# Optimization experiments

Hardware: AMD Instinct MI355X
Metric: run time of the kernel (lower is better)

Reference implementation:

```python
import jax, jax.numpy as jnp
import numpy as np
import math

B = 2
D_MODEL = 2048
L_MAX = 4096
FILTER_ORDER = 64
EMB_DIM = 3
SHORT_K = 3


def setup_inputs() -> dict:
    key = jax.random.key(0)
    ks = jax.random.split(key, 16)
    D = D_MODEL

    def n(k, shape, scale=0.02):
        return jax.random.normal(k, shape, dtype=jnp.float32) * scale

    return {
        "x": jax.random.normal(ks[0], (B, L_MAX, D), dtype=jnp.float32),
        "in_proj_w": n(ks[1], (3 * D, D)),
        "in_proj_b": n(ks[2], (3 * D,)),
        "short_w": n(ks[3], (3 * D, 1, SHORT_K), 0.3),   # depthwise conv weight (O, I/groups=1, K)
        "short_b": n(ks[4], (3 * D,), 0.1),
        "mlp_w0": n(ks[5], (FILTER_ORDER, EMB_DIM), 0.5),
        "mlp_b0": n(ks[6], (FILTER_ORDER,), 0.5),
        "sin_freq": jnp.ones((1, FILTER_ORDER), dtype=jnp.float32),  # Sin module, w=1, shared across MLP layers
        "mlp_w1": n(ks[7], (FILTER_ORDER, FILTER_ORDER), 0.1),
        "mlp_b1": n(ks[8], (FILTER_ORDER,), 0.1),
        "mlp_w2": n(ks[9], (FILTER_ORDER, FILTER_ORDER), 0.1),
        "mlp_b2": n(ks[10], (FILTER_ORDER,), 0.1),
        "mlp_w3": n(ks[11], (D, FILTER_ORDER), 0.1),      # final Linear(order -> d_model, bias=False)
        "filter_bias": jax.random.normal(ks[12], (D,), dtype=jnp.float32),  # HyenaFilter.bias ~ randn
        "out_proj_w": n(ks[13], (D, D)),
        "out_proj_b": n(ks[14], (D,)),
    }


def _pos_emb(L):
    # PositionalEmbedding: t in [0,1], 1 complex band (emb_dim=3 -> bands=1)
    t = jnp.linspace(0.0, 1.0, L)[:, None]               # (L, 1)
    t_resc = jnp.linspace(0.0, L - 1.0, L)
    w = 2.0 * math.pi * t_resc / L                       # (L,)
    bands = (EMB_DIM - 1) // 2
    f = jnp.linspace(1e-4, bands - 1.0, bands)           # (bands,)
    ang = f[None, :] * w[:, None]                        # (L, bands)
    # z = exp(-1j * f * w) -> real = cos, imag = -sin
    z = jnp.concatenate([t, jnp.cos(ang), -jnp.sin(ang)], axis=-1)  # (L, 3)
    return z, t


def _filter_k(L, w0, b0, freq, w1, b1, w2, b2, w3):
    z, t = _pos_emb(L)
    h = jnp.sin(freq * (z @ w0.T + b0))
    h = jnp.sin(freq * (h @ w1.T + b1))
    h = jnp.sin(freq * (h @ w2.T + b2))
    h = h @ w3.T                                         # (L, D)
    # ExponentialModulation: deltas = linspace(log(.01)/1.5, log(.01)/0.3, D)
    max_decay = math.log(0.01) / 0.3
    min_decay = math.log(0.01) / 1.5
    deltas = jnp.linspace(min_decay, max_decay, h.shape[-1])
    decay = jnp.exp(-t * jnp.abs(deltas)[None, :])       # (L, D)
    return (h * decay).T                                 # (D, L)


def _fftconv(u, k, bias):
    # fftconv_ref with gelu=False, no dropout_mask: u (B, D, L), k (D, L), bias (D,)
    L = u.shape[-1]
    n = 2 * L
    k_f = jnp.fft.rfft(k, n=n) / n                       # (D, L+1)
    u_f = jnp.fft.rfft(u, n=n)                           # (B, D, L+1)
    y = jnp.fft.irfft(u_f * k_f, n=n, norm="forward")[..., :L]
    return y + u * bias[:, None]


def reference(x, in_proj_w, in_proj_b, short_w, short_b, mlp_w0, mlp_b0, sin_freq,
              mlp_w1, mlp_b1, mlp_w2, mlp_b2, mlp_w3, filter_bias,
              out_proj_w, out_proj_b):
    Bn, L, D = x.shape
    u = x @ in_proj_w.T + in_proj_b                      # (B, L, 3D)
    u = jnp.transpose(u, (0, 2, 1))                      # (B, 3D, L)
    # depthwise short conv, padding = short_k - 1, truncate to L (causal-ish)
    uc = jax.lax.conv_general_dilated(
        u, short_w, window_strides=(1,),
        padding=[(SHORT_K - 1, SHORT_K - 1)],
        feature_group_count=3 * D,
        dimension_numbers=("NCH", "OIH", "NCH"))
    uc = uc[..., :L] + short_b[None, :, None]
    x0, x1, v = jnp.split(uc, 3, axis=1)                 # each (B, D, L)
    k = _filter_k(L, mlp_w0, mlp_b0, sin_freq, mlp_w1, mlp_b1, mlp_w2, mlp_b2, mlp_w3)
    # order=2 Hyena recurrence: single gated long-conv step
    v = v * x1
    v = _fftconv(v, k, filter_bias)
    y = v * x0                                           # (B, D, L)
    y = jnp.transpose(y, (0, 2, 1))                      # (B, L, D)
    return y @ out_proj_w.T + out_proj_b
```

## Files before the change

kernel.cpp:

```cpp
#include <hip/hip_runtime.h>
#include <hip/hip_bf16.h>
#include <cstdint>
#include <cstddef>

typedef __attribute__((ext_vector_type(8))) short    bf16x8;
typedef __attribute__((ext_vector_type(4))) float    f32x4;
typedef __attribute__((ext_vector_type(8))) unsigned short u16x8;
typedef __attribute__((ext_vector_type(4))) float    f32v4;
typedef __attribute__((ext_vector_type(4))) unsigned short u16v4;

__device__ __forceinline__ float b2f(unsigned short v) {
    return __builtin_bit_cast(float, ((unsigned int)v) << 16);
}
__device__ __forceinline__ unsigned short f2b(float f) {
    unsigned int u = __builtin_bit_cast(unsigned int, f);
    u += 0x7fffu + ((u >> 16) & 1u);
    return (unsigned short)(u >> 16);
}

__device__ __forceinline__ void async16(const void* g, void* l) {
    __builtin_amdgcn_global_load_lds(
        (const __attribute__((address_space(1))) unsigned int*)g,
        (__attribute__((address_space(3))) unsigned int*)l, 16, 0, 0);
}

__global__ __launch_bounds__(256) void cvt_f32_bf16(const float* __restrict__ src,
                                                    unsigned short* __restrict__ dst, int n4) {
    int i = blockIdx.x * blockDim.x + threadIdx.x;
    int stride = gridDim.x * blockDim.x;
    const f32v4* s4 = (const f32v4*)src;
    u16v4* d4 = (u16v4*)dst;
    for (; i < n4; i += stride) {
        f32v4 v = s4[i];
        u16v4 o;
        o.x = f2b(v.x); o.y = f2b(v.y); o.z = f2b(v.z); o.w = f2b(v.w);
        d4[i] = o;
    }
}

template <int MODE>
__global__ __launch_bounds__(512, 1) void gemm256(
    const unsigned short* __restrict__ A,
    const unsigned short* __restrict__ Bw,
    const float* __restrict__ bias,
    void* __restrict__ Cout,
    int M, int N, int K, int Lseq, int CH, int ntn)
{
    constexpr int SMEM_BYTES = (MODE == 1) ? 135168 : 131072;
    __shared__ char smemc[SMEM_BYTES];

    const int tid = threadIdx.x;
    const int w   = tid >> 6;
    const int l   = tid & 63;
    const int wm  = w & 1;
    const int wn  = w >> 1;
    const int quad = l >> 4;
    const int lq   = l & 15;

    int id = blockIdx.x;
    const int q8 = gridDim.x >> 3;
    id = (id & 7) * q8 + (id >> 3);
    const int bx = id % ntn, by = id / ntn;
    const int n0 = bx * 256, m0 = by * 256;

    const int su0 = quad ^ (lq & 7);
    const int su1 = su0 ^ 4;

    uint32_t offAe[2][2], offBe[2][2];
    int dA[2][2], dB[2][2];
    #pragma unroll
    for (int h = 0; h < 2; ++h)
        #pragma unroll
        for (int c = 0; c < 2; ++c) {
            const int Lr = h * 128 + w * 16 + c * 8 + (l >> 3);
            const int gA = ((Lr & 64) << 1) | ((Lr & 128) >> 1) | (Lr & 63);
            const int u  = (l & 7) ^ (l >> 3);
            offAe[h][c] = (uint32_t)(m0 + gA) * (uint32_t)K + (uint32_t)(u * 8);
            offBe[h][c] = (uint32_t)(n0 + Lr) * (uint32_t)K + (uint32_t)(u * 8);
            const int rb = (h * 128 + w * 16 + c * 8) * 128;
            dA[h][c] = rb;
            dB[h][c] = 32768 + rb;
        }

#define STAGE_A(bs, h, tile) do { \
    async16(A + offAe[h][0] + (size_t)(tile) * 64, smemc + ((bs) * 65536 + dA[h][0])); \
    async16(A + offAe[h][1] + (size_t)(tile) * 64, smemc + ((bs) * 65536 + dA[h][1])); \
} while (0)
#define STAGE_B(bs, h, tile) do { \
    async16(Bw + offBe[h][0] + (size_t)(tile) * 64, smemc + ((bs) * 65536 + dB[h][0])); \
    async16(Bw + offBe[h][1] + (size_t)(tile) * 64, smemc + ((bs) * 65536 + dB[h][1])); \
} while (0)

    f32x4 acc[8][4] = {};
    bf16x8 bw[4][2], a[2][2];

#define LDB8(bs) do { \
    _Pragma("unroll") for (int j = 0; j < 4; ++j) { \
        const int Lr = wn * 64 + j * 16 + lq; \
        bw[j][0] = *(const bf16x8*)(smemc + (bs) * 65536 + 32768 + Lr * 128 + su0 * 16); \
        bw[j][1] = *(const bf16x8*)(smemc + (bs) * 65536 + 32768 + Lr * 128 + su1 * 16); \
    } } while (0)
#define LDA4(bs, q) do { \
    _Pragma("unroll") for (int mf = 0; mf < 2; ++mf) { \
        const int g = wm * 128 + (q) * 32 + mf * 16 + lq; \
        const int Lr = ((g & 64) << 1) | ((g & 128) >> 1) | (g & 63); \
        a[mf][0] = *(const bf16x8*)(smemc + (bs) * 65536 + Lr * 128 + su0 * 16); \
        a[mf][1] = *(const bf16x8*)(smemc + (bs) * 65536 + Lr * 128 + su1 * 16); \
    } } while (0)
#define MFMA16(q) do { \
    _Pragma("unroll") for (int mf = 0; mf < 2; ++mf) \
    _Pragma("unroll") for (int j = 0; j < 4; ++j) \
    _Pragma("unroll") for (int kk = 0; kk < 2; ++kk) \
        acc[(q) * 2 + mf][j] = __builtin_amdgcn_mfma_f32_16x16x32_bf16(a[mf][kk], bw[j][kk], acc[(q) * 2 + mf][j], 0, 0, 0); \
} while (0)
#define PHASE_SYNC() do { \
    __builtin_amdgcn_s_barrier(); \
    asm volatile("s_waitcnt lgkmcnt(0)" ::: "memory"); \
    __builtin_amdgcn_sched_barrier(0); \
    __builtin_amdgcn_s_setprio(1); \
} while (0)
#define PHASE_END() do { \
    __builtin_amdgcn_s_setprio(0); \
    __builtin_amdgcn_s_barrier(); \
} while (0)
#define PHASE_END_DRAIN(lastf) do { \
    __builtin_amdgcn_s_setprio(0); \
    if (lastf) asm volatile("s_waitcnt vmcnt(0)" ::: "memory"); \
    else       asm volatile("s_waitcnt vmcnt(6)" ::: "memory"); \
    __builtin_amdgcn_s_barrier(); \
} while (0)

    STAGE_B(0, 0, 0); STAGE_B(0, 1, 0); STAGE_A(0, 0, 0); STAGE_A(0, 1, 0);
    STAGE_B(1, 0, 1); STAGE_B(1, 1, 1); STAGE_A(1, 0, 1);
    asm volatile("s_waitcnt vmcnt(6)" ::: "memory");
    __builtin_amdgcn_s_barrier();

    const int nIt = K >> 7;
    for (int i = 0; i < nIt; ++i) {
        const bool last = (i == nIt - 1);
        const int t0 = 2 * i, t1 = 2 * i + 1;
        LDB8(0); LDA4(0, 0); STAGE_A(1, 1, t1);
        PHASE_SYNC(); MFMA16(0); PHASE_END();
        LDA4(0, 1); if (!last) STAGE_B(0, 0, t0 + 2);
        PHASE_SYNC(); MFMA16(1); PHASE_END();
        LDA4(0, 2); if (!last) STAGE_B(0, 1, t0 + 2);
        PHASE_SYNC(); MFMA16(2); PHASE_END();
        LDA4(0, 3); if (!last) STAGE_A(0, 0, t0 + 2);
        PHASE_SYNC(); MFMA16(3); PHASE_END_DRAIN(last);
        LDB8(1); LDA4(1, 0); if (!last) STAGE_A(0, 1, t0 + 2);
        PHASE_SYNC(); MFMA16(0); PHASE_END();
        LDA4(1, 1); if (!last) STAGE_B(1, 0, t1 + 2);
        PHASE_SYNC(); MFMA16(1); PHASE_END();
        LDA4(1, 2); if (!last) STAGE_B(1, 1, t1 + 2);
        PHASE_SYNC(); MFMA16(2); PHASE_END();
        LDA4(1, 3); if (!last) STAGE_A(1, 0, t1 + 2);
        PHASE_SYNC(); MFMA16(3); PHASE_END_DRAIN(last);
    }

    if (MODE == 0) {
        float* out = (float*)Cout;
        #pragma unroll
        for (int j = 0; j < 4; ++j) {
            const int col = n0 + wn * 64 + j * 16 + lq;
            const float bv = bias[col];
            #pragma unroll
            for (int i8 = 0; i8 < 8; ++i8) {
                const int rowb = m0 + wm * 128 + i8 * 16 + quad * 4;
                f32x4 c = acc[i8][j];
                out[(size_t)(rowb + 0) * N + col] = c.x + bv;
                out[(size_t)(rowb + 1) * N + col] = c.y + bv;
                out[(size_t)(rowb + 2) * N + col] = c.z + bv;
                out[(size_t)(rowb + 3) * N + col] = c.w + bv;
            }
        }
    } else {
        unsigned short* sE = (unsigned short*)smemc;
        __syncthreads();
        #pragma unroll
        for (int j = 0; j < 4; ++j) {
            const int nl = wn * 64 + j * 16 + lq;
            const float bv = bias[n0 + nl];
            #pragma unroll
            for (int i8 = 0; i8 < 8; ++i8) {
                const int ml = wm * 128 + i8 * 16 + quad * 4;
                f32x4 c = acc[i8][j];
                u16v4 pk;
                pk.x = f2b(c.x + bv); pk.y = f2b(c.y + bv);
                pk.z = f2b(c.z + bv); pk.w = f2b(c.w + bv);
                *(u16v4*)&sE[nl * 264 + ml] = pk;
            }
        }
        __syncthreads();
        unsigned short* uo = (unsigned short*)Cout;
        const int bI = m0 >> 12;
        const int l0 = m0 & 4095;
        for (int e = tid; e < 8192; e += 512) {
            const int nl = e >> 5, seg = e & 31;
            u16x8 v = *(const u16x8*)&sE[nl * 264 + seg * 8];
            *(u16x8*)&uo[(size_t)(bI * CH + n0 + nl) * Lseq + l0 + seg * 8] = v;
        }
    }
#undef STAGE_A
#undef STAGE_B
#undef LDB8
#undef LDA4
#undef MFMA16
#undef PHASE_SYNC
#undef PHASE_END
#undef PHASE_END_DRAIN
}

__global__ __launch_bounds__(256) void filter_kernel(
    const float* __restrict__ w0, const float* __restrict__ b0,
    const float* __restrict__ freq,
    const float* __restrict__ w1, const float* __restrict__ b1,
    const float* __restrict__ w2, const float* __restrict__ b2,
    const float* __restrict__ w3, float* __restrict__ kf)
{
    __shared__ float ha[64][64];
    __shared__ float hb[64][64];
    const int tid = threadIdx.x;
    const int l0 = blockIdx.x * 64;
    const int d0 = blockIdx.y * 256;
    const int l  = tid & 63;
    const int lg = l0 + l;
    const float tt = (float)lg * (1.0f / 4095.0f);
    const float wang = 6.283185307179586f * (float)lg * (1.0f / 4096.0f);
    const float a  = 1e-4f * wang;
    const float z0 = tt, z1 = cosf(a), z2 = -sinf(a);

    for (int e = tid; e < 4096; e += 256) {
        const int dim = e >> 6;
        float pre = z0 * w0[dim * 3] + z1 * w0[dim * 3 + 1] + z2 * w0[dim * 3 + 2] + b0[dim];
        ha[dim][l] = sinf(freq[dim] * pre);
    }
    __syncthreads();
    for (int e = tid; e < 4096; e += 256) {
        const int dim = e >> 6;
        float acc = b1[dim];
        #pragma unroll
        for (int jj = 0; jj < 64; ++jj) acc += w1[dim * 64 + jj] * ha[jj][l];
        hb[dim][l] = sinf(freq[dim] * acc);
    }
    __syncthreads();
    for (int e = tid; e < 4096; e += 256) {
        const int dim = e >> 6;
        float acc = b2[dim];
        #pragma unroll
        for (int jj = 0; jj < 64; ++jj) acc += w2[dim * 64 + jj] * hb[jj][l];
        ha[dim][l] = sinf(freq[dim] * acc);
    }
    __syncthreads();
    for (int d = d0 + (tid >> 6); d < d0 + 256; d += 4) {
        float acc = 0.f;
        #pragma unroll
        for (int jj = 0; jj < 64; ++jj) acc += w3[d * 64 + jj] * ha[jj][l];
        const float delta = fabsf(-3.0701134573253944f + (-5.999245642062483e-3f) * (float)d);
        kf[(size_t)d * 4096 + lg] = acc * __expf(-tt * delta);
    }
}

#define PIDX(i) ((i) + (((i) >> 5) << 2))

__device__ __forceinline__ void bfly_f(float& r1, float& i1, float& r2, float& i2, float wr, float wi) {
    float ur = r1, ui = i1, vr = r2, vi = i2;
    r1 = ur + vr; i1 = ui + vi;
    float dr = ur - vr, di = ui - vi;
    r2 = dr * wr - di * wi;
    i2 = dr * wi + di * wr;
}
__device__ __forceinline__ void bfly_i(float& r1, float& i1, float& r2, float& i2, float wr, float wi) {
    float vr = r2 * wr - i2 * wi, vi = r2 * wi + i2 * wr;
    float ur = r1, ui = i1;
    r1 = ur + vr; i1 = ui + vi;
    r2 = ur - vr; i2 = ui - vi;
}

template <int DS, int STR>
__device__ __forceinline__ void fwd_stage(float* re, float* im, int tt) {
    float wr[8], wi[8];
    constexpr float c = -3.14159265358979f / (float)(STR * DS);
    #pragma unroll
    for (int k = 0; k < DS; ++k) __sincosf(c * (float)(tt + STR * k), &wi[k], &wr[k]);
    #pragma unroll
    for (int s = 0; s < 16; ++s)
        if ((s & DS) == 0)
            bfly_f(re[s], im[s], re[s + DS], im[s + DS], wr[s & (DS - 1)], wi[s & (DS - 1)]);
}
template <int DS, int STR>
__device__ __forceinline__ void inv_stage(float* re, float* im, int tt) {
    float wr[8], wi[8];
    constexpr float c = 3.14159265358979f / (float)(STR * DS);
    #pragma unroll
    for (int k = 0; k < DS; ++k) __sincosf(c * (float)(tt + STR * k), &wi[k], &wr[k]);
    #pragma unroll
    for (int s = 0; s < 16; ++s)
        if ((s & DS) == 0)
            bfly_i(re[s], im[s], re[s + DS], im[s + DS], wr[s & (DS - 1)], wi[s & (DS - 1)]);
}

__device__ __forceinline__ void xchg(float* re, float* im, float* fre, float* fim,
                                     int wbase, int wstr, int rbase, int rstr) {
    __syncthreads();
    if (wstr == 1) {
        #pragma unroll
        for (int q = 0; q < 4; ++q) {
            f32x4 vr, vi;
            vr.x = re[4*q+0]; vr.y = re[4*q+1]; vr.z = re[4*q+2]; vr.w = re[4*q+3];
            vi.x = im[4*q+0]; vi.y = im[4*q+1]; vi.z = im[4*q+2]; vi.w = im[4*q+3];
            *(f32x4*)&fre[PIDX(wbase + 4*q)] = vr;
            *(f32x4*)&fim[PIDX(wbase + 4*q)] = vi;
        }
    } else {
        #pragma unroll
        for (int s = 0; s < 16; ++s) {
            const int i = wbase + wstr * s;
            fre[PIDX(i)] = re[s]; fim[PIDX(i)] = im[s];
        }
    }
    __syncthreads();
    if (rstr == 1) {
        #pragma unroll
        for (int q = 0; q < 4; ++q) {
            f32x4 vr = *(const f32x4*)&fre[PIDX(rbase + 4*q)];
            f32x4 vi = *(const f32x4*)&fim[PIDX(rbase + 4*q)];
            re[4*q+0] = vr.x; re[4*q+1] = vr.y; re[4*q+2] = vr.z; re[4*q+3] = vr.w;
            im[4*q+0] = vi.x; im[4*q+1] = vi.y; im[4*q+2] = vi.z; im[4*q+3] = vi.w;
        }
    } else {
        #pragma unroll
        for (int s = 0; s < 16; ++s) {
            const int i = rbase + rstr * s;
            re[s] = fre[PIDX(i)]; im[s] = fim[PIDX(i)];
        }
    }
}

__device__ __forceinline__ void fwd_fft(float* re, float* im, float* fre, float* fim, int t) {
    const int off = t & 31, seg = t >> 5;
    fwd_stage<8, 512>(re, im, t);
    fwd_stage<4, 512>(re, im, t);
    fwd_stage<2, 512>(re, im, t);
    fwd_stage<1, 512>(re, im, t);
    xchg(re, im, fre, fim, t, 512, seg * 512 + off, 32);
    fwd_stage<8, 32>(re, im, off);
    fwd_stage<4, 32>(re, im, off);
    fwd_stage<2, 32>(re, im, off);
    fwd_stage<1, 32>(re, im, off);
    {
        float wr, wi;
        __sincosf(-3.14159265358979f * (float)(off & 15) / 16.0f, &wi, &wr);
        const bool hi = (off & 16) != 0;
        #pragma unroll
        for (int s = 0; s < 16; ++s) {
            float rr = __shfl_xor(re[s], 16);
            float ri = __shfl_xor(im[s], 16);
            if (!hi) { re[s] += rr; im[s] += ri; }
            else {
                float dr = rr - re[s], di = ri - im[s];
                re[s] = dr * wr - di * wi;
                im[s] = dr * wi + di * wr;
            }
        }
    }
    xchg(re, im, fre, fim, seg * 512 + off, 32, 16 * t, 1);
    fwd_stage<8, 1>(re, im, 0);
    fwd_stage<4, 1>(re, im, 0);
    fwd_stage<2, 1>(re, im, 0);
    fwd_stage<1, 1>(re, im, 0);
}

__device__ __forceinline__ void inv_fft(float* re, float* im, float* fre, float* fim, int t) {
    const int off = t & 31, seg = t >> 5;
    inv_stage<1, 1>(re, im, 0);
    inv_stage<2, 1>(re, im, 0);
    inv_stage<4, 1>(re, im, 0);
    inv_stage<8, 1>(re, im, 0);
    xchg(re, im, fre, fim, 16 * t, 1, seg * 512 + off, 32);
    {
        float wr, wi;
        __sincosf(3.14159265358979f * (float)(off & 15) / 16.0f, &wi, &wr);
        const bool hi = (off & 16) != 0;
        #pragma unroll
        for (int s = 0; s < 16; ++s) {
            float rr = __shfl_xor(re[s], 16);
            float ri = __shfl_xor(im[s], 16);
            if (!hi) {
                float vr = rr * wr - ri * wi, vi = rr * wi + ri * wr;
                re[s] += vr; im[s] += vi;
            } else {
                float vr = re[s] * wr - im[s] * wi, vi = re[s] * wi + im[s] * wr;
                re[s] = rr - vr; im[s] = ri - vi;
            }
        }
    }
    inv_stage<1, 32>(re, im, off);
    inv_stage<2, 32>(re, im, off);
    inv_stage<4, 32>(re, im, off);
    inv_stage<8, 32>(re, im, off);
    xchg(re, im, fre, fim, seg * 512 + off, 32, t, 512);
    inv_stage<1, 512>(re, im, t);
    inv_stage<2, 512>(re, im, t);
    inv_stage<4, 512>(re, im, t);
    inv_stage<8, 512>(re, im, t);
}

__global__ __launch_bounds__(512, 2) void kfft_kernel(
    const float* __restrict__ kf,
    float* __restrict__ kspec)
{
    __shared__ __align__(16) float fre[9216];
    __shared__ __align__(16) float fim[9216];
    const int t = threadIdx.x;
    const int d = blockIdx.x;
    float kr[16], ki[16];
    #pragma unroll
    for (int s = 0; s < 16; ++s) {
        kr[s] = (s < 8) ? kf[(size_t)d * 4096 + t + 512 * s] : 0.f;
        ki[s] = 0.f;
    }
    fwd_fft(kr, ki, fre, fim, t);
    f32x4* kv = (f32x4*)kspec + (size_t)d * 4096 + t;
    #pragma unroll
    for (int q = 0; q < 8; ++q) {
        f32x4 o;
        o.x = kr[2 * q]; o.y = ki[2 * q];
        o.z = kr[2 * q + 1]; o.w = ki[2 * q + 1];
        kv[q * 512] = o;
    }
}

__device__ __forceinline__ void conv8(const unsigned short* __restrict__ row, int lb,
                                      float W0, float W1, float W2, float BB,
                                      float* __restrict__ out) {
    u16x8 v8 = *(const u16x8*)(row + lb);
    float f[8];
    #pragma unroll
    for (int j = 0; j < 8; ++j) f[j] = b2f(v8[j]);
    const float fm1 = (lb >= 1) ? b2f(row[lb - 1]) : 0.f;
    const float fm2 = (lb >= 2) ? b2f(row[lb - 2]) : 0.f;
    out[0] = W0 * fm2 + W1 * fm1 + W2 * f[0] + BB;
    out[1] = W0 * fm1 + W1 * f[0] + W2 * f[1] + BB;
    #pragma unroll
    for (int j = 2; j < 8; ++j) out[j] = W0 * f[j - 2] + W1 * f[j - 1] + W2 * f[j] + BB;
}

__global__ __launch_bounds__(512, 2) void hyena_fft_kernel(
    const unsigned short* __restrict__ u,
    const float* __restrict__ kspec,
    const float* __restrict__ sw,
    const float* __restrict__ sbv,
    const float* __restrict__ fbias,
    unsigned short* __restrict__ zb)
{
    __shared__ __align__(16) float fre[9216];
    __shared__ __align__(16) float fim[9216];
    const int t = threadIdx.x;
    const int d = blockIdx.x;
    const int lb = t << 3;

    const int c0 = d, c1 = 2048 + d, c2 = 4096 + d;
    const float w00 = sw[c0*3+0], w01 = sw[c0*3+1], w02 = sw[c0*3+2], bb0 = sbv[c0];
    const float w10 = sw[c1*3+0], w11 = sw[c1*3+1], w12 = sw[c1*3+2], bb1 = sbv[c1];
    const float w20 = sw[c2*3+0], w21 = sw[c2*3+1], w22 = sw[c2*3+2], bb2 = sbv[c2];
    const float fb = fbias[d];

    float vgc[2][8], x0c[2][8];
    #pragma unroll
    for (int b = 0; b < 2; ++b) {
        const size_t base = (size_t)b * 6144 * 4096;
        float a_[8], e_[8], g_[8];
        conv8(u + base + (size_t)c0 * 4096, lb, w00, w01, w02, bb0, a_);
        conv8(u + base + (size_t)c1 * 4096, lb, w10, w11, w12, bb1, e_);
        conv8(u + base + (size_t)c2 * 4096, lb, w20, w21, w22, bb2, g_);
        #pragma unroll
        for (int j = 0; j < 8; ++j) { x0c[b][j] = a_[j]; vgc[b][j] = g_[j] * e_[j]; }
    }

    #pragma unroll
    for (int q = 0; q < 2; ++q) {
        f32x4 vr, vi;
        vr.x = vgc[0][4*q+0]; vr.y = vgc[0][4*q+1]; vr.z = vgc[0][4*q+2]; vr.w = vgc[0][4*q+3];
        vi.x = vgc[1][4*q+0]; vi.y = vgc[1][4*q+1]; vi.z = vgc[1][4*q+2]; vi.w = vgc[1][4*q+3];
        *(f32x4*)&fre[PIDX(lb + 4*q)] = vr;
        *(f32x4*)&fim[PIDX(lb + 4*q)] = vi;
    }
    __syncthreads();
    float xr[16], xi[16];
    #pragma unroll
    for (int s = 0; s < 8; ++s) {
        xr[s] = fre[PIDX(t + (s << 9))];
        xi[s] = fim[PIDX(t + (s << 9))];
    }
    #pragma unroll
    for (int s = 8; s < 16; ++s) { xr[s] = 0.f; xi[s] = 0.f; }

    fwd_fft(xr, xi, fre, fim, t);
    {
        const f32x4* kv = (const f32x4*)kspec + (size_t)d * 4096 + t;
        f32x4 kk[8];
        #pragma unroll
        for (int q = 0; q < 8; ++q) kk[q] = kv[q * 512];
        #pragma unroll
        for (int q = 0; q < 8; ++q) {
            float cr = xr[2 * q], ci = xi[2 * q];
            xr[2 * q] = cr * kk[q].x - ci * kk[q].y;
            xi[2 * q] = cr * kk[q].y + ci * kk[q].x;
            cr = xr[2 * q + 1]; ci = xi[2 * q + 1];
            xr[2 * q + 1] = cr * kk[q].z - ci * kk[q].w;
            xi[2 * q + 1] = cr * kk[q].w + ci * kk[q].z;
        }
    }
    inv_fft(xr, xi, fre, fim, t);

    __syncthreads();
    #pragma unroll
    for (int s = 0; s < 8; ++s) {
        fre[PIDX(t + (s << 9))] = xr[s];
        fim[PIDX(t + (s << 9))] = xi[s];
    }
    __syncthreads();
    float yr[8], yi[8];
    #pragma unroll
    for (int q = 0; q < 2; ++q) {
        f32x4 vr = *(const f32x4*)&fre[PIDX(lb + 4*q)];
        f32x4 vi = *(const f32x4*)&fim[PIDX(lb + 4*q)];
        yr[4*q+0] = vr.x; yr[4*q+1] = vr.y; yr[4*q+2] = vr.z; yr[4*q+3] = vr.w;
        yi[4*q+0] = vi.x; yi[4*q+1] = vi.y; yi[4*q+2] = vi.z; yi[4*q+3] = vi.w;
    }
    const float inv_n = 1.0f / 8192.0f;
    u16x8 z0v, z1v;
    #pragma unroll
    for (int j = 0; j < 8; ++j) {
        z0v[j] = (unsigned short)f2b((yr[j] * inv_n + vgc[0][j] * fb) * x0c[0][j]);
        z1v[j] = (unsigned short)f2b((yi[j] * inv_n + vgc[1][j] * fb) * x0c[1][j]);
    }
    *(u16x8*)&zb[(size_t)d * 4096 + lb]          = z0v;
    *(u16x8*)&zb[(size_t)(2048 + d) * 4096 + lb] = z1v;
}

__global__ __launch_bounds__(256) void transpose_kernel(const unsigned short* __restrict__ zb,
                                                        unsigned short* __restrict__ zt)
{
    __shared__ unsigned int tile[64][65];
    const int l0 = blockIdx.x * 64, d0 = blockIdx.y * 64, b = blockIdx.z;
    const int tid = threadIdx.x;
    for (int e = tid; e < 4096; e += 256) {
        const int r = e >> 6, c = e & 63;
        tile[r][c] = zb[(size_t)(b * 2048 + d0 + r) * 4096 + l0 + c];
    }
    __syncthreads();
    for (int e = tid; e < 4096; e += 256) {
        const int r = e >> 6, c = e & 63;
        zt[(size_t)(b * 4096 + l0 + r) * 2048 + d0 + c] = (unsigned short)tile[c][r];
    }
}

extern "C" void kernel_launch(void* const* d_in, const int* in_sizes, int n_in,
                              void* d_out, int out_size, void* d_ws, size_t ws_size,
                              hipStream_t stream)
{
    const float* x   = (const float*)d_in[0];
    const float* ipw = (const float*)d_in[1];
    const float* ipb = (const float*)d_in[2];
    const float* sw  = (const float*)d_in[3];
    const float* sb  = (const float*)d_in[4];
    const float* w0  = (const float*)d_in[5];
    const float* b0  = (const float*)d_in[6];
    const float* fr  = (const float*)d_in[7];
    const float* w1  = (const float*)d_in[8];
    const float* b1  = (const float*)d_in[9];
    const float* w2  = (const float*)d_in[10];
    const float* b2  = (const float*)d_in[11];
    const float* w3  = (const float*)d_in[12];
    const float* fb  = (const float*)d_in[13];
    const float* opw = (const float*)d_in[14];
    const float* opb = (const float*)d_in[15];
    float* out = (float*)d_out;

    char* ws = (char*)d_ws;
    unsigned short* xb    = (unsigned short*)ws;
    unsigned short* wbi   = (unsigned short*)(ws + 33554432);
    float*          kspec = (float*)ws;
    unsigned short* ztb   = (unsigned short*)ws;
    unsigned short* wbo   = (unsigned short*)(ws + 33554432);
    unsigned short* ub    = (unsigned short*)(ws + 134217728);
    float*          kf    = (float*)(ws + 234881024);
    unsigned short* zbm   = (unsigned short*)(ws + 234881024);

    cvt_f32_bf16<<<1024, 256, 0, stream>>>(x,   xb,  16777216 / 4);
    cvt_f32_bf16<<<1024, 256, 0, stream>>>(ipw, wbi, 12582912 / 4);

    gemm256<1><<<768, 512, 0, stream>>>(xb, wbi, ipb, ub, 8192, 6144, 2048, 4096, 6144, 24);

    filter_kernel<<<dim3(64, 8), 256, 0, stream>>>(w0, b0, fr, w1, b1, w2, b2, w3, kf);

    kfft_kernel<<<2048, 512, 0, stream>>>(kf, kspec);

    hyena_fft_kernel<<<2048, 512, 0, stream>>>(ub, kspec, sw, sb, fb, zbm);

    transpose_kernel<<<dim3(64, 32, 2), 256, 0, stream>>>(zbm, ztb);

    cvt_f32_bf16<<<512,  256, 0, stream>>>(opw, wbo, 4194304 / 4);

    gemm256<0><<<256, 512, 0, stream>>>(ztb, wbo, opb, out, 8192, 2048, 2048, 4096, 2048, 8);
}
```

Measured before the change: 749.9 us.

## Remap GEMM block order, use constant FFT twiddles, merge conversion kernels

Replaces the GEMM block-ID remap with a hardcoded grouping. Each XCD-strided group of blocks now covers a compact 4-row by 8-column patch of output tiles, which should improve L2 reuse of A and B panels. The last four radix-2 stages of the forward and inverse FFTs now read compile-time twiddle constants instead of computing sin/cos at runtime. The two fp32-to-bf16 conversion launches become one kernel. The new tile mapping is only valid for these exact grid shapes (ntn of 8 or 24).

```diff
diff --git a/kernel.cpp b/kernel.cpp
--- a/kernel.cpp
+++ b/kernel.cpp
@@ -22,6 +22,24 @@
     __builtin_amdgcn_global_load_lds(
         (const __attribute__((address_space(1))) unsigned int*)g,
         (__attribute__((address_space(3))) unsigned int*)l, 16, 0, 0);
+}
+
+__global__ __launch_bounds__(256) void cvt2_f32_bf16(
+    const float* __restrict__ srcA, unsigned short* __restrict__ dstA, int n4A,
+    const float* __restrict__ srcB, unsigned short* __restrict__ dstB, int n4B) {
+    int i = blockIdx.x * blockDim.x + threadIdx.x;
+    int stride = gridDim.x * blockDim.x;
+    const int nTot = n4A + n4B;
+    for (; i < nTot; i += stride) {
+        const bool inA = (i < n4A);
+        const f32v4* s4 = inA ? (const f32v4*)srcA : (const f32v4*)srcB;
+        u16v4* d4 = inA ? (u16v4*)dstA : (u16v4*)dstB;
+        const int k = inA ? i : (i - n4A);
+        f32v4 v = s4[k];
+        u16v4 o;
+        o.x = f2b(v.x); o.y = f2b(v.y); o.z = f2b(v.z); o.w = f2b(v.w);
+        d4[k] = o;
+    }
 }
 
 __global__ __launch_bounds__(256) void cvt_f32_bf16(const float* __restrict__ src,
@@ -57,10 +75,11 @@
     const int quad = l >> 4;
     const int lq   = l & 15;
 
-    int id = blockIdx.x;
-    const int q8 = gridDim.x >> 3;
-    id = (id & 7) * q8 + (id >> 3);
-    const int bx = id % ntn, by = id / ntn;
+    const int bid = blockIdx.x;
+    const int x  = bid & 7;
+    const int j  = bid >> 3;
+    const int bx = (j & 7) + 8 * (j >> 5);
+    const int by = (x << 2) | ((j >> 3) & 3);
     const int n0 = bx * 256, m0 = by * 256;
 
     const int su0 = quad ^ (lq & 7);
@@ -95,10 +114,10 @@
     bf16x8 bw[4][2], a[2][2];
 
 #define LDB8(bs) do { \
-    _Pragma("unroll") for (int j = 0; j < 4; ++j) { \
-        const int Lr = wn * 64 + j * 16 + lq; \
-        bw[j][0] = *(const bf16x8*)(smemc + (bs) * 65536 + 32768 + Lr * 128 + su0 * 16); \
-        bw[j][1] = *(const bf16x8*)(smemc + (bs) * 65536 + 32768 + Lr * 128 + su1 * 16); \
+    _Pragma("unroll") for (int jj = 0; jj < 4; ++jj) { \
+        const int Lr = wn * 64 + jj * 16 + lq; \
+        bw[jj][0] = *(const bf16x8*)(smemc + (bs) * 65536 + 32768 + Lr * 128 + su0 * 16); \
+        bw[jj][1] = *(const bf16x8*)(smemc + (bs) * 65536 + 32768 + Lr * 128 + su1 * 16); \
     } } while (0)
 #define LDA4(bs, q) do { \
     _Pragma("unroll") for (int mf = 0; mf < 2; ++mf) { \
@@ -109,9 +128,9 @@
     } } while (0)
 #define MFMA16(q) do { \
     _Pragma("unroll") for (int mf = 0; mf < 2; ++mf) \
-    _Pragma("unroll") for (int j = 0; j < 4; ++j) \
+    _Pragma("unroll") for (int jj = 0; jj < 4; ++jj) \
     _Pragma("unroll") for (int kk = 0; kk < 2; ++kk) \
-        acc[(q) * 2 + mf][j] = __builtin_amdgcn_mfma_f32_16x16x32_bf16(a[mf][kk], bw[j][kk], acc[(q) * 2 + mf][j], 0, 0, 0); \
+        acc[(q) * 2 + mf][jj] = __builtin_amdgcn_mfma_f32_16x16x32_bf16(a[mf][kk], bw[jj][kk], acc[(q) * 2 + mf][jj], 0, 0, 0); \
 } while (0)
 #define PHASE_SYNC() do { \
     __builtin_amdgcn_s_barrier(); \
@@ -160,13 +179,13 @@
     if (MODE == 0) {
         float* out = (float*)Cout;
         #pragma unroll
-        for (int j = 0; j < 4; ++j) {
-            const int col = n0 + wn * 64 + j * 16 + lq;
+        for (int jj = 0; jj < 4; ++jj) {
+            const int col = n0 + wn * 64 + jj * 16 + lq;
             const float bv = bias[col];
             #pragma unroll
             for (int i8 = 0; i8 < 8; ++i8) {
                 const int rowb = m0 + wm * 128 + i8 * 16 + quad * 4;
-                f32x4 c = acc[i8][j];
+                f32x4 c = acc[i8][jj];
                 out[(size_t)(rowb + 0) * N + col] = c.x + bv;
                 out[(size_t)(rowb + 1) * N + col] = c.y + bv;
                 out[(size_t)(rowb + 2) * N + col] = c.z + bv;
@@ -177,13 +196,13 @@
         unsigned short* sE = (unsigned short*)smemc;
         __syncthreads();
         #pragma unroll
-        for (int j = 0; j < 4; ++j) {
-            const int nl = wn * 64 + j * 16 + lq;
+        for (int jj = 0; jj < 4; ++jj) {
+            const int nl = wn * 64 + jj * 16 + lq;
             const float bv = bias[n0 + nl];
             #pragma unroll
             for (int i8 = 0; i8 < 8; ++i8) {
                 const int ml = wm * 128 + i8 * 16 + quad * 4;
-                f32x4 c = acc[i8][j];
+                f32x4 c = acc[i8][jj];
                 u16v4 pk;
                 pk.x = f2b(c.x + bv); pk.y = f2b(c.y + bv);
                 pk.z = f2b(c.z + bv); pk.w = f2b(c.w + bv);
@@ -299,6 +318,29 @@
             bfly_i(re[s], im[s], re[s + DS], im[s + DS], wr[s & (DS - 1)], wi[s & (DS - 1)]);
 }
 
+__device__ constexpr float TW8C[8] = { 1.f,  0.9238795325112867f,  0.7071067811865476f,  0.3826834323650898f,
+                                       0.f, -0.3826834323650898f, -0.7071067811865476f, -0.9238795325112867f };
+__device__ constexpr float TW8S[8] = { 0.f,  0.3826834323650898f,  0.7071067811865476f,  0.9238795325112867f,
+                                       1.f,  0.9238795325112867f,  0.7071067811865476f,  0.3826834323650898f };
+template <int DS>
+__device__ __forceinline__ void fwd_stageC(float* re, float* im) {
+    #pragma unroll
+    for (int s = 0; s < 16; ++s)
+        if ((s & DS) == 0) {
+            const int k = (s & (DS - 1)) * (8 / DS);
+            bfly_f(re[s], im[s], re[s + DS], im[s + DS], TW8C[k], -TW8S[k]);
+        }
+}
+template <int DS>
+__device__ __forceinline__ void inv_stageC(float* re, float* im) {
+    #pragma unroll
+    for (int s = 0; s < 16; ++s)
+        if ((s & DS) == 0) {
+            const int k = (s & (DS - 1)) * (8 / DS);
+            bfly_i(re[s], im[s], re[s + DS], im[s + DS], TW8C[k], TW8S[k]);
+        }
+}
+
 __device__ __forceinline__ void xchg(float* re, float* im, float* fre, float* fim,
                                      int wbase, int wstr, int rbase, int rstr) {
     __syncthreads();
@@ -364,18 +406,18 @@
         }
     }
     xchg(re, im, fre, fim, seg * 512 + off, 32, 16 * t, 1);
-    fwd_stage<8, 1>(re, im, 0);
-    fwd_stage<4, 1>(re, im, 0);
-    fwd_stage<2, 1>(re, im, 0);
-    fwd_stage<1, 1>(re, im, 0);
+    fwd_stageC<8>(re, im);
+    fwd_stageC<4>(re, im);
+    fwd_stageC<2>(re, im);
+    fwd_stageC<1>(re, im);
 }
 
 __device__ __forceinline__ void inv_fft(float* re, float* im, float* fre, float* fim, int t) {
     const int off = t & 31, seg = t >> 5;
-    inv_stage<1, 1>(re, im, 0);
-    inv_stage<2, 1>(re, im, 0);
-    inv_stage<4, 1>(re, im, 0);
-    inv_stage<8, 1>(re, im, 0);
+    inv_stageC<1>(re, im);
+    inv_stageC<2>(re, im);
+    inv_stageC<4>(re, im);
+    inv_stageC<8>(re, im);
     xchg(re, im, fre, fim, 16 * t, 1, seg * 512 + off, 32);
     {
         float wr, wi;
@@ -588,8 +630,7 @@
     float*          kf    = (float*)(ws + 234881024);
     unsigned short* zbm   = (unsigned short*)(ws + 234881024);
 
-    cvt_f32_bf16<<<1024, 256, 0, stream>>>(x,   xb,  16777216 / 4);
-    cvt_f32_bf16<<<1024, 256, 0, stream>>>(ipw, wbi, 12582912 / 4);
+    cvt2_f32_bf16<<<1536, 256, 0, stream>>>(x, xb, 16777216 / 4, ipw, wbi, 12582912 / 4);
 
     gemm256<1><<<768, 512, 0, stream>>>(xb, wbi, ipb, ub, 8192, 6144, 2048, 4096, 6144, 24);
 
```

Result: faster. 733.3 us (-2.2%).
